# Optimization experiments

Hardware: AMD Instinct MI355X
Metric: run time of the kernel (lower is better)

The kernel has to match this reference:

```python
import jax, jax.numpy as jnp
import numpy as np

HUGE = 1e31  # ops.HUGE_INT
EPS = 1e-20

NUM_ENT, NUM_REL = 100000, 400
ENT_D, REL_D, HIST_D = 256, 256, 512
ACT_D = ENT_D + REL_D          # 512
IN_D = ENT_D + HIST_D + REL_D  # 1024
B, A = 512, 256


def setup_inputs() -> dict:
    key = jax.random.key(0)
    ks = jax.random.split(key, 10)
    s = 0.02
    return {
        "current_entity": jax.random.randint(ks[0], (B,), 0, NUM_ENT),
        "query_relation": jax.random.randint(ks[1], (B,), 0, NUM_REL),
        "encoded_history": jax.random.normal(ks[2], (B, HIST_D), jnp.float32),
        "r_space": jax.random.randint(ks[3], (B, A), 0, NUM_REL),
        "e_space": jax.random.randint(ks[4], (B, A), 0, NUM_ENT),
        "action_mask": jax.random.randint(ks[5], (B, A), 0, 2).astype(jnp.int32),
        "entity_emb": jax.random.normal(ks[6], (NUM_ENT, ENT_D), jnp.float32) * s,
        "relation_emb": jax.random.normal(ks[7], (NUM_REL, REL_D), jnp.float32) * s,
        "W1": jax.random.normal(ks[8], (IN_D, ACT_D), jnp.float32) * s,
        "b1": jnp.zeros((ACT_D,), jnp.float32),
        "W2": jax.random.normal(ks[9], (ACT_D, ACT_D), jnp.float32) * s,
        "b2": jnp.zeros((ACT_D,), jnp.float32),
    }


def reference(current_entity, query_relation, encoded_history, r_space, e_space,
              action_mask, entity_emb, relation_emb, W1, b1, W2, b2):
    # encode_history: [E(cur) | lstm hidden | R(query)] -> [B, IN_D]
    X = jnp.concatenate([entity_emb[current_entity], encoded_history,
                         relation_emb[query_relation]], axis=-1)
    # policy MLP (dropout = identity in eval)
    X2 = jax.nn.relu(X @ W1 + b1) @ W2 + b2          # [B, ACT_D]
    # per-action embeddings: concat(rel, ent) -> [B, A, ACT_D]
    A_emb = jnp.concatenate([relation_emb[r_space], entity_emb[e_space]], axis=-1)
    mask = action_mask.astype(X2.dtype)
    scores = jnp.einsum('bad,bd->ba', A_emb, X2) - (1.0 - mask) * HUGE
    action_dist = jax.nn.softmax(scores, axis=-1)    # [B, A]
    entropy = -jnp.sum(action_dist * jnp.log(action_dist + EPS), axis=-1)  # [B]
    return action_dist, entropy
```

## Files before the change

kernel.cpp:

```cpp
#include <hip/hip_runtime.h>
#include <hip/hip_bf16.h>

#define ENT_D 256
#define REL_D 256
#define HIST_D 512
#define ACT_DD 512
#define IN_DD 1024
#define BB 512
#define AA 256

typedef short bf16x8 __attribute__((ext_vector_type(8)));
typedef float floatx4 __attribute__((ext_vector_type(4)));

__device__ __forceinline__ unsigned short f2bf(float f) {
    unsigned u = __builtin_bit_cast(unsigned, f);
    return (unsigned short)((u + 0x7fffu + ((u >> 16) & 1u)) >> 16);
}


__global__ __launch_bounds__(256) void pack_kernel(
    const int* __restrict__ cur, const int* __restrict__ qrel,
    const float* __restrict__ hist,
    const float* __restrict__ ent_emb, const float* __restrict__ rel_emb,
    const float* __restrict__ W1, const float* __restrict__ W2,
    unsigned short* __restrict__ W1p, unsigned short* __restrict__ W2p,
    unsigned short* __restrict__ Xp)
{
    const int wid  = blockIdx.x * 4 + (threadIdx.x >> 6);
    const int lane = threadIdx.x & 63;
    const int l15  = lane & 15;
    const int quad = lane >> 4;
    unsigned short v[8];

    if (wid < 1024) {
        const int t = wid, nt = t >> 5, kt = t & 31;
        const int n = nt * 16 + l15, k0 = kt * 32 + quad * 8;
#pragma unroll
        for (int j = 0; j < 8; ++j) v[j] = f2bf(W1[(size_t)(k0 + j) * ACT_DD + n]);
        *(bf16x8*)(W1p + ((size_t)t * 64 + lane) * 8) = *(bf16x8*)v;
    } else if (wid < 1536) {
        const int t = wid - 1024, nt = t >> 4, kt = t & 15;
        const int n = nt * 16 + l15, k0 = kt * 32 + quad * 8;
#pragma unroll
        for (int j = 0; j < 8; ++j) v[j] = f2bf(W2[(size_t)(k0 + j) * ACT_DD + n]);
        *(bf16x8*)(W2p + ((size_t)t * 64 + lane) * 8) = *(bf16x8*)v;
    } else {
        const int t = wid - 1536, mt = t >> 5, kt = t & 31;
        const int m = mt * 16 + l15, k0 = kt * 32 + quad * 8;
        const float* src;
        if (k0 < ENT_D)            src = ent_emb + (size_t)cur[m] * ENT_D + k0;
        else if (k0 < ENT_D + HIST_D) src = hist + (size_t)m * HIST_D + (k0 - ENT_D);
        else                       src = rel_emb + (size_t)qrel[m] * REL_D + (k0 - ENT_D - HIST_D);
        float4 a = *(const float4*)src, b = *(const float4*)(src + 4);
        v[0]=f2bf(a.x); v[1]=f2bf(a.y); v[2]=f2bf(a.z); v[3]=f2bf(a.w);
        v[4]=f2bf(b.x); v[5]=f2bf(b.y); v[6]=f2bf(b.z); v[7]=f2bf(b.w);
        *(bf16x8*)(Xp + ((size_t)t * 64 + lane) * 8) = *(bf16x8*)v;
    }
}

__global__ __launch_bounds__(256) void gemm1_kernel(
    const unsigned short* __restrict__ Xp, const unsigned short* __restrict__ W1p,
    const float* __restrict__ b1, unsigned short* __restrict__ Hp)
{
    __shared__ unsigned short sH[1024];
    const int mt = blockIdx.x, wave = threadIdx.x >> 6, lane = threadIdx.x & 63;
    const int nt = blockIdx.y * 4 + wave;

    const bf16x8* Av = (const bf16x8*)Xp  + (size_t)mt * 32 * 64 + lane;
    const bf16x8* Bv = (const bf16x8*)W1p + (size_t)nt * 32 * 64 + lane;
    floatx4 acc = {0.f, 0.f, 0.f, 0.f};
#pragma unroll 8
    for (int kt = 0; kt < 32; ++kt)
        acc = __builtin_amdgcn_mfma_f32_16x16x32_bf16(Av[kt * 64], Bv[kt * 64], acc, 0, 0, 0);

    const int col  = nt * 16 + (lane & 15);
    const float bj = b1[col];
    const int n_loc = wave * 16 + (lane & 15);
    const int tile_loc = n_loc >> 5, quad2 = (n_loc & 31) >> 3, j2 = n_loc & 7;
#pragma unroll
    for (int reg = 0; reg < 4; ++reg) {
        const int row = (lane >> 4) * 4 + reg;
        const float h = fmaxf(acc[reg] + bj, 0.f);
        sH[tile_loc * 512 + (row + 16 * quad2) * 8 + j2] = f2bf(h);
    }
    __syncthreads();
    const int h = threadIdx.x * 4;
    const int tl = h >> 9, rest = h & 511;
    const size_t dst = ((size_t)(mt * 16 + blockIdx.y * 2 + tl) * 512 + rest);
    *(uint2*)(Hp + dst) = *(const uint2*)(sH + h);
}

__global__ __launch_bounds__(256) void gemm2_kernel(
    const unsigned short* __restrict__ Hp, const unsigned short* __restrict__ W2p,
    const float* __restrict__ b2, float* __restrict__ X2)
{
    const int mt = blockIdx.x, wave = threadIdx.x >> 6, lane = threadIdx.x & 63;
    const int nt = blockIdx.y * 4 + wave;

    const bf16x8* Av = (const bf16x8*)Hp  + (size_t)mt * 16 * 64 + lane;
    const bf16x8* Bv = (const bf16x8*)W2p + (size_t)nt * 16 * 64 + lane;
    floatx4 acc = {0.f, 0.f, 0.f, 0.f};
#pragma unroll
    for (int kt = 0; kt < 16; ++kt)
        acc = __builtin_amdgcn_mfma_f32_16x16x32_bf16(Av[kt * 64], Bv[kt * 64], acc, 0, 0, 0);

    const int col = nt * 16 + (lane & 15);
    const float bj = b2[col];
#pragma unroll
    for (int reg = 0; reg < 4; ++reg) {
        const int m = mt * 16 + (lane >> 4) * 4 + reg;
        X2[(size_t)m * ACT_DD + col] = acc[reg] + bj;
    }
}

__global__ __launch_bounds__(512) void score_softmax_kernel(
    const float* __restrict__ X2,
    const int* __restrict__ r_space, const int* __restrict__ e_space,
    const int* __restrict__ amask,
    const float* __restrict__ ent_emb, const float* __restrict__ rel_emb,
    float* __restrict__ dist, float* __restrict__ ent_out)
{
    __shared__ __align__(16) float x2s[ACT_DD];
    __shared__ float sc[AA];
    __shared__ int   list[AA];
    __shared__ int   wcnt[4];
    __shared__ int   n_u_s;
    __shared__ float red[8];

    const int b = blockIdx.x, tid = threadIdx.x;
    const int wave = tid >> 6, lane = tid & 63;

    x2s[tid] = X2[(size_t)b * ACT_DD + tid];

    int m = 0;
    unsigned long long bal = 0;
    int pre = 0;
    if (tid < AA) {
        m = amask[b * AA + tid];
        sc[tid] = 0.0f;
    }
    if (wave < 4) {
        bal = __ballot(m != 0);
        pre = __popcll(bal & ((1ull << lane) - 1ull));
        if (lane == 0) wcnt[wave] = __popcll(bal);
    }
    __syncthreads();

    if (wave < 4) {
        int off = 0;
#pragma unroll
        for (int w = 0; w < 4; ++w) if (w < wave) off += wcnt[w];
        if (m != 0) list[off + pre] = tid;
        if (tid == 0) n_u_s = wcnt[0] + wcnt[1] + wcnt[2] + wcnt[3];
    }
    __syncthreads();

    const int n_u = n_u_s;
    const int padded = (n_u + 63) & ~63;
    if (tid < padded - n_u) list[n_u + tid] = list[0];
    __syncthreads();

    const float4 xr = ((const float4*)&x2s[0])[lane];
    const float4 xe = ((const float4*)&x2s[REL_D])[lane];

    for (int base = wave * 8; base < padded; base += 64) {
        int ai[8], ir[8], ie[8];
#pragma unroll
        for (int i = 0; i < 8; ++i) ai[i] = list[base + i];
#pragma unroll
        for (int i = 0; i < 8; ++i) {
            ir[i] = r_space[b * AA + ai[i]];
            ie[i] = e_space[b * AA + ai[i]];
        }
        float4 r4[8], e4[8];
#pragma unroll
        for (int i = 0; i < 8; ++i)
            r4[i] = ((const float4*)(rel_emb + (size_t)ir[i] * REL_D))[lane];
#pragma unroll
        for (int i = 0; i < 8; ++i)
            e4[i] = ((const float4*)(ent_emb + (size_t)ie[i] * ENT_D))[lane];

        float p[8];
#pragma unroll
        for (int i = 0; i < 8; ++i)
            p[i] = r4[i].x * xr.x + r4[i].y * xr.y + r4[i].z * xr.z + r4[i].w * xr.w
                 + e4[i].x * xe.x + e4[i].y * xe.y + e4[i].z * xe.z + e4[i].w * xe.w;
#pragma unroll
        for (int off = 32; off > 0; off >>= 1) {
#pragma unroll
            for (int i = 0; i < 8; ++i) p[i] += __shfl_xor(p[i], off, 64);
        }
        if (lane == 0) {
#pragma unroll
            for (int i = 0; i < 8; ++i) sc[ai[i]] = p[i];
        }
    }
    __syncthreads();

    float s = -3.0e38f;
    if (tid < AA) s = (m != 0) ? sc[tid] : (sc[tid] - 1e31f);
    float v = s;
#pragma unroll
    for (int off = 32; off > 0; off >>= 1) v = fmaxf(v, __shfl_xor(v, off, 64));
    if (lane == 0) red[wave] = v;
    __syncthreads();
    float mx = red[0];
#pragma unroll
    for (int w = 1; w < 8; ++w) mx = fmaxf(mx, red[w]);
    __syncthreads();

    const float e = (tid < AA) ? __expf(s - mx) : 0.0f;
    v = e;
#pragma unroll
    for (int off = 32; off > 0; off >>= 1) v += __shfl_xor(v, off, 64);
    if (lane == 0) red[wave] = v;
    __syncthreads();
    float sum = red[0];
#pragma unroll
    for (int w = 1; w < 8; ++w) sum += red[w];
    __syncthreads();

    const float p = e / sum;
    if (tid < AA) dist[(size_t)b * AA + tid] = p;

    v = (tid < AA) ? p * __logf(p + 1e-20f) : 0.0f;
#pragma unroll
    for (int off = 32; off > 0; off >>= 1) v += __shfl_xor(v, off, 64);
    if (lane == 0) red[wave] = v;
    __syncthreads();
    if (tid == 0) {
        float t = red[0];
#pragma unroll
        for (int w = 1; w < 8; ++w) t += red[w];
        ent_out[b] = -t;
    }
}

extern "C" void kernel_launch(void* const* d_in, const int* in_sizes, int n_in,
                              void* d_out, int out_size, void* d_ws, size_t ws_size,
                              hipStream_t stream) {
    const int*   cur      = (const int*)d_in[0];
    const int*   qrel     = (const int*)d_in[1];
    const float* hist     = (const float*)d_in[2];
    const int*   r_space  = (const int*)d_in[3];
    const int*   e_space  = (const int*)d_in[4];
    const int*   amask    = (const int*)d_in[5];
    const float* ent_emb  = (const float*)d_in[6];
    const float* rel_emb  = (const float*)d_in[7];
    const float* W1       = (const float*)d_in[8];
    const float* b1       = (const float*)d_in[9];
    const float* W2       = (const float*)d_in[10];
    const float* b2       = (const float*)d_in[11];

    float* dist    = (float*)d_out;
    float* entropy = dist + (size_t)BB * AA;

    char* w = (char*)d_ws;
    unsigned short* W1p = (unsigned short*)(w);
    unsigned short* W2p = (unsigned short*)(w + (1u << 20));
    unsigned short* Xp  = (unsigned short*)(w + (3u << 19));
    unsigned short* Hp  = (unsigned short*)(w + (5u << 19));
    float*          X2  = (float*)(w + (6u << 19));

    pack_kernel<<<640, 256, 0, stream>>>(cur, qrel, hist, ent_emb, rel_emb, W1, W2, W1p, W2p, Xp);
    gemm1_kernel<<<dim3(32, 8), 256, 0, stream>>>(Xp, W1p, b1, Hp);
    gemm2_kernel<<<dim3(32, 8), 256, 0, stream>>>(Hp, W2p, b2, X2);
    score_softmax_kernel<<<512, 512, 0, stream>>>(X2, r_space, e_space, amask,
                                                  ent_emb, rel_emb, dist, entropy);
}
```

Before: 184.8 us.

## Fuse pack, both GEMMs and softmax into one cooperative kernel with grid syncs

Merges the four launches (weight/input packing, GEMM1, GEMM2, score+softmax) into a single cooperative kernel of 512 blocks of 256 threads, separated by grid-wide syncs. This removes launch gaps and inter-kernel drain between the small stages. The softmax stage now uses 256 threads per batch row instead of 512, so each wave gathers more actions. The grid syncs add a barrier cost, and cooperative launch requires all 512 blocks to be resident at once.

Result: slower. 500.7 us (+171.0%).

```diff
diff --git a/kernel.cpp b/kernel.cpp
--- a/kernel.cpp
+++ b/kernel.cpp
@@ -1,5 +1,8 @@
 #include <hip/hip_runtime.h>
 #include <hip/hip_bf16.h>
+#include <hip/hip_cooperative_groups.h>
+
+namespace cg = cooperative_groups;
 
 #define ENT_D 256
 #define REL_D 256
@@ -17,136 +20,128 @@
     return (unsigned short)((u + 0x7fffu + ((u >> 16) & 1u)) >> 16);
 }
 
-
-__global__ __launch_bounds__(256) void pack_kernel(
+__global__ __launch_bounds__(256, 2) void fused_kernel(
     const int* __restrict__ cur, const int* __restrict__ qrel,
     const float* __restrict__ hist,
-    const float* __restrict__ ent_emb, const float* __restrict__ rel_emb,
-    const float* __restrict__ W1, const float* __restrict__ W2,
-    unsigned short* __restrict__ W1p, unsigned short* __restrict__ W2p,
-    unsigned short* __restrict__ Xp)
-{
-    const int wid  = blockIdx.x * 4 + (threadIdx.x >> 6);
-    const int lane = threadIdx.x & 63;
-    const int l15  = lane & 15;
-    const int quad = lane >> 4;
-    unsigned short v[8];
-
-    if (wid < 1024) {
-        const int t = wid, nt = t >> 5, kt = t & 31;
-        const int n = nt * 16 + l15, k0 = kt * 32 + quad * 8;
-#pragma unroll
-        for (int j = 0; j < 8; ++j) v[j] = f2bf(W1[(size_t)(k0 + j) * ACT_DD + n]);
-        *(bf16x8*)(W1p + ((size_t)t * 64 + lane) * 8) = *(bf16x8*)v;
-    } else if (wid < 1536) {
-        const int t = wid - 1024, nt = t >> 4, kt = t & 15;
-        const int n = nt * 16 + l15, k0 = kt * 32 + quad * 8;
-#pragma unroll
-        for (int j = 0; j < 8; ++j) v[j] = f2bf(W2[(size_t)(k0 + j) * ACT_DD + n]);
-        *(bf16x8*)(W2p + ((size_t)t * 64 + lane) * 8) = *(bf16x8*)v;
-    } else {
-        const int t = wid - 1536, mt = t >> 5, kt = t & 31;
-        const int m = mt * 16 + l15, k0 = kt * 32 + quad * 8;
-        const float* src;
-        if (k0 < ENT_D)            src = ent_emb + (size_t)cur[m] * ENT_D + k0;
-        else if (k0 < ENT_D + HIST_D) src = hist + (size_t)m * HIST_D + (k0 - ENT_D);
-        else                       src = rel_emb + (size_t)qrel[m] * REL_D + (k0 - ENT_D - HIST_D);
-        float4 a = *(const float4*)src, b = *(const float4*)(src + 4);
-        v[0]=f2bf(a.x); v[1]=f2bf(a.y); v[2]=f2bf(a.z); v[3]=f2bf(a.w);
-        v[4]=f2bf(b.x); v[5]=f2bf(b.y); v[6]=f2bf(b.z); v[7]=f2bf(b.w);
-        *(bf16x8*)(Xp + ((size_t)t * 64 + lane) * 8) = *(bf16x8*)v;
-    }
-}
-
-__global__ __launch_bounds__(256) void gemm1_kernel(
-    const unsigned short* __restrict__ Xp, const unsigned short* __restrict__ W1p,
-    const float* __restrict__ b1, unsigned short* __restrict__ Hp)
-{
-    __shared__ unsigned short sH[1024];
-    const int mt = blockIdx.x, wave = threadIdx.x >> 6, lane = threadIdx.x & 63;
-    const int nt = blockIdx.y * 4 + wave;
-
-    const bf16x8* Av = (const bf16x8*)Xp  + (size_t)mt * 32 * 64 + lane;
-    const bf16x8* Bv = (const bf16x8*)W1p + (size_t)nt * 32 * 64 + lane;
-    floatx4 acc = {0.f, 0.f, 0.f, 0.f};
-#pragma unroll 8
-    for (int kt = 0; kt < 32; ++kt)
-        acc = __builtin_amdgcn_mfma_f32_16x16x32_bf16(Av[kt * 64], Bv[kt * 64], acc, 0, 0, 0);
-
-    const int col  = nt * 16 + (lane & 15);
-    const float bj = b1[col];
-    const int n_loc = wave * 16 + (lane & 15);
-    const int tile_loc = n_loc >> 5, quad2 = (n_loc & 31) >> 3, j2 = n_loc & 7;
-#pragma unroll
-    for (int reg = 0; reg < 4; ++reg) {
-        const int row = (lane >> 4) * 4 + reg;
-        const float h = fmaxf(acc[reg] + bj, 0.f);
-        sH[tile_loc * 512 + (row + 16 * quad2) * 8 + j2] = f2bf(h);
-    }
-    __syncthreads();
-    const int h = threadIdx.x * 4;
-    const int tl = h >> 9, rest = h & 511;
-    const size_t dst = ((size_t)(mt * 16 + blockIdx.y * 2 + tl) * 512 + rest);
-    *(uint2*)(Hp + dst) = *(const uint2*)(sH + h);
-}
-
-__global__ __launch_bounds__(256) void gemm2_kernel(
-    const unsigned short* __restrict__ Hp, const unsigned short* __restrict__ W2p,
-    const float* __restrict__ b2, float* __restrict__ X2)
-{
-    const int mt = blockIdx.x, wave = threadIdx.x >> 6, lane = threadIdx.x & 63;
-    const int nt = blockIdx.y * 4 + wave;
-
-    const bf16x8* Av = (const bf16x8*)Hp  + (size_t)mt * 16 * 64 + lane;
-    const bf16x8* Bv = (const bf16x8*)W2p + (size_t)nt * 16 * 64 + lane;
-    floatx4 acc = {0.f, 0.f, 0.f, 0.f};
-#pragma unroll
-    for (int kt = 0; kt < 16; ++kt)
-        acc = __builtin_amdgcn_mfma_f32_16x16x32_bf16(Av[kt * 64], Bv[kt * 64], acc, 0, 0, 0);
-
-    const int col = nt * 16 + (lane & 15);
-    const float bj = b2[col];
-#pragma unroll
-    for (int reg = 0; reg < 4; ++reg) {
-        const int m = mt * 16 + (lane >> 4) * 4 + reg;
-        X2[(size_t)m * ACT_DD + col] = acc[reg] + bj;
-    }
-}
-
-__global__ __launch_bounds__(512) void score_softmax_kernel(
-    const float* __restrict__ X2,
     const int* __restrict__ r_space, const int* __restrict__ e_space,
     const int* __restrict__ amask,
     const float* __restrict__ ent_emb, const float* __restrict__ rel_emb,
+    const float* __restrict__ W1, const float* __restrict__ b1,
+    const float* __restrict__ W2, const float* __restrict__ b2,
+    unsigned short* __restrict__ W1p, unsigned short* __restrict__ W2p,
+    unsigned short* __restrict__ Xp, unsigned short* __restrict__ Hp,
+    float* __restrict__ X2,
     float* __restrict__ dist, float* __restrict__ ent_out)
 {
+    cg::grid_group grid = cg::this_grid();
+
+    __shared__ unsigned short sH[1024];
     __shared__ __align__(16) float x2s[ACT_DD];
     __shared__ float sc[AA];
     __shared__ int   list[AA];
     __shared__ int   wcnt[4];
     __shared__ int   n_u_s;
-    __shared__ float red[8];
-
-    const int b = blockIdx.x, tid = threadIdx.x;
+    __shared__ float red[4];
+
+    const int blk  = blockIdx.x;
+    const int tid  = threadIdx.x;
     const int wave = tid >> 6, lane = tid & 63;
-
-    x2s[tid] = X2[(size_t)b * ACT_DD + tid];
-
-    int m = 0;
-    unsigned long long bal = 0;
-    int pre = 0;
-    if (tid < AA) {
-        m = amask[b * AA + tid];
-        sc[tid] = 0.0f;
-    }
-    if (wave < 4) {
-        bal = __ballot(m != 0);
-        pre = __popcll(bal & ((1ull << lane) - 1ull));
-        if (lane == 0) wcnt[wave] = __popcll(bal);
-    }
-    __syncthreads();
-
-    if (wave < 4) {
+    const int l15  = lane & 15, quad = lane >> 4;
+
+    for (int wid = blk * 4 + wave; wid < 2560; wid += 2048) {
+        unsigned short v[8];
+        if (wid < 1024) {
+            const int t = wid, nt = t >> 5, kt = t & 31;
+            const int n = nt * 16 + l15, k0 = kt * 32 + quad * 8;
+#pragma unroll
+            for (int j = 0; j < 8; ++j) v[j] = f2bf(W1[(size_t)(k0 + j) * ACT_DD + n]);
+            *(bf16x8*)(W1p + ((size_t)t * 64 + lane) * 8) = *(bf16x8*)v;
+        } else if (wid < 1536) {
+            const int t = wid - 1024, nt = t >> 4, kt = t & 15;
+            const int n = nt * 16 + l15, k0 = kt * 32 + quad * 8;
+#pragma unroll
+            for (int j = 0; j < 8; ++j) v[j] = f2bf(W2[(size_t)(k0 + j) * ACT_DD + n]);
+            *(bf16x8*)(W2p + ((size_t)t * 64 + lane) * 8) = *(bf16x8*)v;
+        } else {
+            const int t = wid - 1536, mt = t >> 5, kt = t & 31;
+            const int m = mt * 16 + l15, k0 = kt * 32 + quad * 8;
+            const float* src;
+            if (k0 < ENT_D)               src = ent_emb + (size_t)cur[m] * ENT_D + k0;
+            else if (k0 < ENT_D + HIST_D) src = hist + (size_t)m * HIST_D + (k0 - ENT_D);
+            else                          src = rel_emb + (size_t)qrel[m] * REL_D + (k0 - ENT_D - HIST_D);
+            float4 a = *(const float4*)src, b = *(const float4*)(src + 4);
+            v[0]=f2bf(a.x); v[1]=f2bf(a.y); v[2]=f2bf(a.z); v[3]=f2bf(a.w);
+            v[4]=f2bf(b.x); v[5]=f2bf(b.y); v[6]=f2bf(b.z); v[7]=f2bf(b.w);
+            *(bf16x8*)(Xp + ((size_t)t * 64 + lane) * 8) = *(bf16x8*)v;
+        }
+    }
+    __threadfence();
+    grid.sync();
+
+    if (blk < 256) {
+        const int mt = blk >> 3, by = blk & 7;
+        const int nt = by * 4 + wave;
+        const bf16x8* Av = (const bf16x8*)Xp  + (size_t)mt * 32 * 64 + lane;
+        const bf16x8* Bv = (const bf16x8*)W1p + (size_t)nt * 32 * 64 + lane;
+        floatx4 acc = {0.f, 0.f, 0.f, 0.f};
+#pragma unroll 8
+        for (int kt = 0; kt < 32; ++kt)
+            acc = __builtin_amdgcn_mfma_f32_16x16x32_bf16(Av[kt * 64], Bv[kt * 64], acc, 0, 0, 0);
+
+        const int col = nt * 16 + l15;
+        const float bj = b1[col];
+        const int n_loc = wave * 16 + l15;
+        const int tile_loc = n_loc >> 5, quad2 = (n_loc & 31) >> 3, j2 = n_loc & 7;
+#pragma unroll
+        for (int reg = 0; reg < 4; ++reg) {
+            const int row = quad * 4 + reg;
+            const float h = fmaxf(acc[reg] + bj, 0.f);
+            sH[tile_loc * 512 + (row + 16 * quad2) * 8 + j2] = f2bf(h);
+        }
+        __syncthreads();
+        const int h = tid * 4;
+        const int tl = h >> 9, rest = h & 511;
+        const size_t dst = ((size_t)(mt * 16 + by * 2 + tl) * 512 + rest);
+        *(uint2*)(Hp + dst) = *(const uint2*)(sH + h);
+    }
+    __threadfence();
+    grid.sync();
+
+    if (blk >= 256) {
+        const int bb = blk - 256;
+        const int mt = bb >> 3, by = bb & 7;
+        const int nt = by * 4 + wave;
+        const bf16x8* Av = (const bf16x8*)Hp  + (size_t)mt * 16 * 64 + lane;
+        const bf16x8* Bv = (const bf16x8*)W2p + (size_t)nt * 16 * 64 + lane;
+        floatx4 acc = {0.f, 0.f, 0.f, 0.f};
+#pragma unroll
+        for (int kt = 0; kt < 16; ++kt)
+            acc = __builtin_amdgcn_mfma_f32_16x16x32_bf16(Av[kt * 64], Bv[kt * 64], acc, 0, 0, 0);
+
+        const int col = nt * 16 + l15;
+        const float bj = b2[col];
+#pragma unroll
+        for (int reg = 0; reg < 4; ++reg) {
+            const int m = mt * 16 + quad * 4 + reg;
+            X2[(size_t)m * ACT_DD + col] = acc[reg] + bj;
+        }
+    }
+    __threadfence();
+    grid.sync();
+
+    const int b = blk;
+
+    x2s[tid]       = X2[(size_t)b * ACT_DD + tid];
+    x2s[tid + 256] = X2[(size_t)b * ACT_DD + tid + 256];
+
+    const int m = amask[b * AA + tid];
+    sc[tid] = 0.0f;
+    const unsigned long long bal = __ballot(m != 0);
+    const int pre = __popcll(bal & ((1ull << lane) - 1ull));
+    if (lane == 0) wcnt[wave] = __popcll(bal);
+    __syncthreads();
+
+    {
         int off = 0;
 #pragma unroll
         for (int w = 0; w < 4; ++w) if (w < wave) off += wcnt[w];
@@ -156,14 +151,14 @@
     __syncthreads();
 
     const int n_u = n_u_s;
-    const int padded = (n_u + 63) & ~63;
+    const int padded = (n_u + 31) & ~31;
     if (tid < padded - n_u) list[n_u + tid] = list[0];
     __syncthreads();
 
     const float4 xr = ((const float4*)&x2s[0])[lane];
     const float4 xe = ((const float4*)&x2s[REL_D])[lane];
 
-    for (int base = wave * 8; base < padded; base += 64) {
+    for (int base = wave * 8; base < padded; base += 32) {
         int ai[8], ir[8], ie[8];
 #pragma unroll
         for (int i = 0; i < 8; ++i) ai[i] = list[base + i];
@@ -197,43 +192,33 @@
     }
     __syncthreads();
 
-    float s = -3.0e38f;
-    if (tid < AA) s = (m != 0) ? sc[tid] : (sc[tid] - 1e31f);
+    const float s = (m != 0) ? sc[tid] : (sc[tid] - 1e31f);
     float v = s;
 #pragma unroll
     for (int off = 32; off > 0; off >>= 1) v = fmaxf(v, __shfl_xor(v, off, 64));
     if (lane == 0) red[wave] = v;
     __syncthreads();
-    float mx = red[0];
-#pragma unroll
-    for (int w = 1; w < 8; ++w) mx = fmaxf(mx, red[w]);
-    __syncthreads();
-
-    const float e = (tid < AA) ? __expf(s - mx) : 0.0f;
+    const float mx = fmaxf(fmaxf(red[0], red[1]), fmaxf(red[2], red[3]));
+    __syncthreads();
+
+    const float e = __expf(s - mx);
     v = e;
 #pragma unroll
     for (int off = 32; off > 0; off >>= 1) v += __shfl_xor(v, off, 64);
     if (lane == 0) red[wave] = v;
     __syncthreads();
-    float sum = red[0];
-#pragma unroll
-    for (int w = 1; w < 8; ++w) sum += red[w];
+    const float sum = red[0] + red[1] + red[2] + red[3];
     __syncthreads();
 
     const float p = e / sum;
-    if (tid < AA) dist[(size_t)b * AA + tid] = p;
-
-    v = (tid < AA) ? p * __logf(p + 1e-20f) : 0.0f;
+    dist[(size_t)b * AA + tid] = p;
+
+    v = p * __logf(p + 1e-20f);
 #pragma unroll
     for (int off = 32; off > 0; off >>= 1) v += __shfl_xor(v, off, 64);
     if (lane == 0) red[wave] = v;
     __syncthreads();
-    if (tid == 0) {
-        float t = red[0];
-#pragma unroll
-        for (int w = 1; w < 8; ++w) t += red[w];
-        ent_out[b] = -t;
-    }
+    if (tid == 0) ent_out[b] = -(red[0] + red[1] + red[2] + red[3]);
 }
 
 extern "C" void kernel_launch(void* const* d_in, const int* in_sizes, int n_in,
@@ -262,9 +247,14 @@
     unsigned short* Hp  = (unsigned short*)(w + (5u << 19));
     float*          X2  = (float*)(w + (6u << 19));
 
-    pack_kernel<<<640, 256, 0, stream>>>(cur, qrel, hist, ent_emb, rel_emb, W1, W2, W1p, W2p, Xp);
-    gemm1_kernel<<<dim3(32, 8), 256, 0, stream>>>(Xp, W1p, b1, Hp);
-    gemm2_kernel<<<dim3(32, 8), 256, 0, stream>>>(Hp, W2p, b2, X2);
-    score_softmax_kernel<<<512, 512, 0, stream>>>(X2, r_space, e_space, amask,
-                                                  ent_emb, rel_emb, dist, entropy);
+    void* args[] = {
+        (void*)&cur, (void*)&qrel, (void*)&hist,
+        (void*)&r_space, (void*)&e_space, (void*)&amask,
+        (void*)&ent_emb, (void*)&rel_emb,
+        (void*)&W1, (void*)&b1, (void*)&W2, (void*)&b2,
+        (void*)&W1p, (void*)&W2p, (void*)&Xp, (void*)&Hp, (void*)&X2,
+        (void*)&dist, (void*)&entropy,
+    };
+    hipLaunchCooperativeKernel((void*)fused_kernel, dim3(512), dim3(256),
+                               args, 0, stream);
 }
```
